# Performance work log

Measured on AMD Instinct MI355X. Metric: run time of the kernel, lower is better.

Reference implementation:

```python
import jax, jax.numpy as jnp
import numpy as np

B, L, H, D = 4, 2048, 16, 64
C = H * D
KERNEL_SIZES = (3, 7, 15, 31)
INIT_STD = 0.02


def _make_filter(key, k):
    # identity (Dirac delta at last tap) + gaussian noise, matching torch init
    filt = jnp.zeros((C, 1, k), dtype=jnp.float32).at[:, 0, -1].set(1.0)
    return filt + INIT_STD * jax.random.normal(key, (C, 1, k), dtype=jnp.float32)


def setup_inputs() -> dict:
    key = jax.random.key(0)
    kx, k3, k7, k15, k31 = jax.random.split(key, 5)
    return {
        "x": jax.random.normal(kx, (B, L, H, D), dtype=jnp.float32),
        "filt3": _make_filter(k3, 3),
        "filt7": _make_filter(k7, 7),
        "filt15": _make_filter(k15, 15),
        "filt31": _make_filter(k31, 31),
    }


def _causal_dwconv(x_flat, filt):
    # x_flat: [b, C, L], filt: [C, 1, k]; causal left-pad of k-1, groups=C
    k = filt.shape[-1]
    return jax.lax.conv_general_dilated(
        x_flat, filt,
        window_strides=(1,),
        padding=[(k - 1, 0)],
        feature_group_count=C,
        dimension_numbers=("NCH", "OIH", "NCH"),
    )


def reference(x, filt3, filt7, filt15, filt31):
    b, l, h, d = x.shape
    # b l h d -> b (h d) l
    x_flat = x.reshape(b, l, h * d).transpose(0, 2, 1)
    outs = []
    for filt in (filt3, filt7, filt15, filt31):
        y = _causal_dwconv(x_flat, filt)          # [b, C, l]
        outs.append(y.transpose(0, 2, 1).reshape(b, l, h, d))
    return tuple(outs)
```

## Files before the change

### kernel.cpp

```cpp
#include <hip/hip_runtime.h>

constexpr int B = 4;
constexpr int L = 2048;
constexpr int C = 1024;
constexpr int TL = 32;
constexpr int KMAX = 31;
constexpr int HIST = KMAX - 1;


__global__ __launch_bounds__(256)
void dwfir_kernel(const float* __restrict__ x,
                  const float* __restrict__ f3,
                  const float* __restrict__ f7,
                  const float* __restrict__ f15,
                  const float* __restrict__ f31,
                  float* __restrict__ out)
{
    const int tile = blockIdx.x;
    const int c    = blockIdx.y * 256 + threadIdx.x;
    const int b    = blockIdx.z;
    const int l0   = tile * TL;

    float w3[3], w7[7], w15[15], w31[31];
#pragma unroll
    for (int j = 0; j < 3;  ++j) w3[j]  = f3 [c * 3  + j];
#pragma unroll
    for (int j = 0; j < 7;  ++j) w7[j]  = f7 [c * 7  + j];
#pragma unroll
    for (int j = 0; j < 15; ++j) w15[j] = f15[c * 15 + j];
#pragma unroll
    for (int j = 0; j < 31; ++j) w31[j] = f31[c * 31 + j];

    float xs[TL + HIST];
    const float* xb = x + ((size_t)b * L) * C + c;
#pragma unroll
    for (int m = 0; m < TL + HIST; ++m) {
        const int li = l0 - HIST + m;
        xs[m] = (li >= 0) ? xb[(size_t)li * C] : 0.0f;
    }

    const size_t plane   = (size_t)B * L * C;
    const size_t outBase = ((size_t)b * L + l0) * C + c;

#pragma unroll
    for (int i = 0; i < TL; ++i) {
        float y31 = 0.f, y15 = 0.f, y7 = 0.f, y3 = 0.f;
#pragma unroll
        for (int j = 0; j < 31; ++j) y31 = fmaf(w31[j], xs[i + j],      y31);
#pragma unroll
        for (int j = 0; j < 15; ++j) y15 = fmaf(w15[j], xs[16 + i + j], y15);
#pragma unroll
        for (int j = 0; j < 7;  ++j) y7  = fmaf(w7[j],  xs[24 + i + j], y7);
#pragma unroll
        for (int j = 0; j < 3;  ++j) y3  = fmaf(w3[j],  xs[28 + i + j], y3);

        const size_t o = outBase + (size_t)i * C;
        out[o]             = y3;
        out[o +     plane] = y7;
        out[o + 2 * plane] = y15;
        out[o + 3 * plane] = y31;
    }
}

extern "C" void kernel_launch(void* const* d_in, const int* in_sizes, int n_in,
                              void* d_out, int out_size, void* d_ws, size_t ws_size,
                              hipStream_t stream) {
    const float* x   = (const float*)d_in[0];
    const float* f3  = (const float*)d_in[1];
    const float* f7  = (const float*)d_in[2];
    const float* f15 = (const float*)d_in[3];
    const float* f31 = (const float*)d_in[4];
    float* out = (float*)d_out;

    dim3 grid(L / TL, C / 256, B);
    dim3 block(256);
    dwfir_kernel<<<grid, block, 0, stream>>>(x, f3, f7, f15, f31, out);
}
```

Measured before the change: 176.9 us.

## Stage input tile in shared memory with float4 loads and sliding register window

Each block now loads a 158x64 tile of x (128 output rows plus the 30-row causal history) into LDS with vectorized float4 loads. Four sub-groups of 64 threads each compute 32 output rows from a sliding register window. This cuts the redundant history reloads from global memory (30 extra rows per 32 outputs before, 30 per 128 now). Outputs use nontemporal stores to avoid polluting the cache. In exchange the kernel adds LDS traffic, a block barrier and register shuffling of the window.

```diff
diff --git a/kernel.cpp b/kernel.cpp
--- a/kernel.cpp
+++ b/kernel.cpp
@@ -1,12 +1,15 @@
 #include <hip/hip_runtime.h>
 
-constexpr int B = 4;
-constexpr int L = 2048;
-constexpr int C = 1024;
-constexpr int TL = 32;
+
+constexpr int B    = 4;
+constexpr int L    = 2048;
+constexpr int C    = 1024;
 constexpr int KMAX = 31;
 constexpr int HIST = KMAX - 1;
-
+constexpr int LT   = 128;
+constexpr int CB   = 64;
+constexpr int ROWS = LT + HIST;
+constexpr int SUB  = 32;
 
 __global__ __launch_bounds__(256)
 void dwfir_kernel(const float* __restrict__ x,
@@ -16,49 +19,70 @@
                   const float* __restrict__ f31,
                   float* __restrict__ out)
 {
-    const int tile = blockIdx.x;
-    const int c    = blockIdx.y * 256 + threadIdx.x;
-    const int b    = blockIdx.z;
-    const int l0   = tile * TL;
+    __shared__ float smem[ROWS][CB];
+
+    const int tid   = threadIdx.x;
+    const int l0    = blockIdx.x * LT;
+    const int cbase = blockIdx.y * CB;
+    const int b     = blockIdx.z;
+
+    const int c = tid & (CB - 1);
+    const int s = tid >> 6;
+    const int cg = cbase + c;
 
     float w3[3], w7[7], w15[15], w31[31];
 #pragma unroll
-    for (int j = 0; j < 3;  ++j) w3[j]  = f3 [c * 3  + j];
+    for (int j = 0; j < 3;  ++j) w3[j]  = f3 [cg * 3  + j];
 #pragma unroll
-    for (int j = 0; j < 7;  ++j) w7[j]  = f7 [c * 7  + j];
+    for (int j = 0; j < 7;  ++j) w7[j]  = f7 [cg * 7  + j];
 #pragma unroll
-    for (int j = 0; j < 15; ++j) w15[j] = f15[c * 15 + j];
+    for (int j = 0; j < 15; ++j) w15[j] = f15[cg * 15 + j];
 #pragma unroll
-    for (int j = 0; j < 31; ++j) w31[j] = f31[c * 31 + j];
+    for (int j = 0; j < 31; ++j) w31[j] = f31[cg * 31 + j];
 
-    float xs[TL + HIST];
-    const float* xb = x + ((size_t)b * L) * C + c;
+    const float* xb = x + ((size_t)b * L) * C + cbase;
+    for (int p = tid; p < ROWS * 16; p += 256) {
+        const int row  = p >> 4;
+        const int col4 = (p & 15) * 4;
+        const int l    = l0 - HIST + row;
+        float4 v = make_float4(0.f, 0.f, 0.f, 0.f);
+        if (l >= 0)
+            v = *reinterpret_cast<const float4*>(xb + (size_t)l * C + col4);
+        *reinterpret_cast<float4*>(&smem[row][col4]) = v;
+    }
+    __syncthreads();
+
+    const int r0 = s * SUB;
+    float win[KMAX];
 #pragma unroll
-    for (int m = 0; m < TL + HIST; ++m) {
-        const int li = l0 - HIST + m;
-        xs[m] = (li >= 0) ? xb[(size_t)li * C] : 0.0f;
-    }
+    for (int m = 0; m < KMAX; ++m) win[m] = smem[r0 + m][c];
 
     const size_t plane   = (size_t)B * L * C;
-    const size_t outBase = ((size_t)b * L + l0) * C + c;
+    const size_t outBase = ((size_t)b * L + l0 + s * SUB) * C + cg;
 
 #pragma unroll
-    for (int i = 0; i < TL; ++i) {
+    for (int i = 0; i < SUB; ++i) {
         float y31 = 0.f, y15 = 0.f, y7 = 0.f, y3 = 0.f;
 #pragma unroll
-        for (int j = 0; j < 31; ++j) y31 = fmaf(w31[j], xs[i + j],      y31);
+        for (int j = 0; j < 31; ++j) y31 = fmaf(w31[j], win[j],      y31);
 #pragma unroll
-        for (int j = 0; j < 15; ++j) y15 = fmaf(w15[j], xs[16 + i + j], y15);
+        for (int j = 0; j < 15; ++j) y15 = fmaf(w15[j], win[16 + j], y15);
 #pragma unroll
-        for (int j = 0; j < 7;  ++j) y7  = fmaf(w7[j],  xs[24 + i + j], y7);
+        for (int j = 0; j < 7;  ++j) y7  = fmaf(w7[j],  win[24 + j], y7);
 #pragma unroll
-        for (int j = 0; j < 3;  ++j) y3  = fmaf(w3[j],  xs[28 + i + j], y3);
+        for (int j = 0; j < 3;  ++j) y3  = fmaf(w3[j],  win[28 + j], y3);
 
         const size_t o = outBase + (size_t)i * C;
-        out[o]             = y3;
-        out[o +     plane] = y7;
-        out[o + 2 * plane] = y15;
-        out[o + 3 * plane] = y31;
+        __builtin_nontemporal_store(y3,  &out[o]);
+        __builtin_nontemporal_store(y7,  &out[o + plane]);
+        __builtin_nontemporal_store(y15, &out[o + 2 * plane]);
+        __builtin_nontemporal_store(y31, &out[o + 3 * plane]);
+
+        if (i < SUB - 1) {
+#pragma unroll
+            for (int m = 0; m < KMAX - 1; ++m) win[m] = win[m + 1];
+            win[KMAX - 1] = smem[r0 + i + KMAX][c];
+        }
     }
 }
 
@@ -72,7 +96,7 @@
     const float* f31 = (const float*)d_in[4];
     float* out = (float*)d_out;
 
-    dim3 grid(L / TL, C / 256, B);
+    dim3 grid(L / LT, C / CB, B);
     dim3 block(256);
     dwfir_kernel<<<grid, block, 0, stream>>>(x, f3, f7, f15, f31, out);
 }
```

Measured after the change: 173.3 us. -2.0%, faster.
